# Performance work log

Measured on AMD Instinct MI355X. Metric: run time of the kernel, lower is better.

Reference implementation:

```python
import jax, jax.numpy as jnp
import numpy as np

B, C, H, W_IMG = 4, 4, 512, 512
OUT_CH = 256
POS_NUM = 512
NEG_NUM = 512
M_MARGIN = 0.5
TAU = 0.1
EPS = 1e-8


def setup_inputs() -> dict:
    key = jax.random.key(0)
    k1, k2, k3, k4, k5, k6 = jax.random.split(key, 6)
    d1_fegc = jax.random.normal(k1, (B, C, H, W_IMG), dtype=jnp.float32)
    p_fegc = jax.random.uniform(k2, (B, 1, H, W_IMG), dtype=jnp.float32)
    p_pre = jax.random.uniform(k3, (B, 3, H, W_IMG), dtype=jnp.float32)
    gt = (jax.random.uniform(k4, (B, 1, H, W_IMG)) < 0.5).astype(jnp.float32)
    # parameters of the nn.Linear(in_channel, out_channel)
    W = jax.random.normal(k5, (OUT_CH, C), dtype=jnp.float32) / np.sqrt(C)
    b_fc = jax.random.normal(k6, (OUT_CH,), dtype=jnp.float32) * 0.01
    return {"d1_fegc": d1_fegc, "p_fegc": p_fegc, "p_pre": p_pre, "gt": gt, "W": W, "b_fc": b_fc}


def _sample_idx(mask_flat, key, n):
    # randomized fixed-size sampling of n indices where mask is True
    # (replaces torch.nonzero + randperm with a jit-friendly top-k over random scores)
    score = jnp.where(mask_flat, jax.random.uniform(key, mask_flat.shape), -jnp.inf)
    _, idx = jax.lax.top_k(score, n)
    return idx


def reference(d1_fegc, p_fegc, p_pre, gt, W, b_fc):
    b, c, h, w = d1_fegc.shape
    P = POS_NUM * b
    N = NEG_NUM * b
    # p_overlap channel 3: fegc foreground AND pre argmax-class 0
    fegc_fg = p_fegc[:, 0] >= 0.5                       # [b,h,w]
    pre_cls0 = jnp.argmax(p_pre, axis=1) == 0           # [b,h,w]
    pre_region = fegc_fg & pre_cls0                     # [b,h,w]
    gt_fg = gt[:, 0] > 0.5                              # [b,h,w]
    pos_mask = (pre_region & gt_fg).reshape(-1)         # [b*h*w]
    neg_mask = (pre_region & ~gt_fg).reshape(-1)        # [b*h*w]
    # per-pixel feature vectors from d1_fegc
    feats = d1_fegc.transpose(0, 2, 3, 1).reshape(-1, c)  # [b*h*w, c]
    skey = jax.random.key(42)
    kp, kn = jax.random.split(skey)
    pos_idx = _sample_idx(pos_mask, kp, P)
    neg_idx = _sample_idx(neg_mask, kn, N)
    pts = jnp.concatenate([feats[pos_idx], feats[neg_idx]], axis=0)  # [P+N, c]
    proj = pts @ W.T + b_fc                                           # [P+N, out]
    # F.cosine_similarity with eps=1e-8 norm clamping
    norm = jnp.maximum(jnp.linalg.norm(proj, axis=-1, keepdims=True), EPS)
    normed = proj / norm
    cos_sim = normed @ normed.T                                       # [P+N, P+N]
    T = P + N
    label = jnp.ones((T, T), dtype=cos_sim.dtype)
    label = label.at[:P, P:].set(0.0).at[P:, :P].set(0.0)
    s = cos_sim / TAU
    lam = (1.0 - label) * jnp.square(s) + label * jnp.square(jnp.maximum(M_MARGIN - s, 0.0))
    lam = lam * (1.0 - jnp.eye(T, dtype=lam.dtype))                   # mask self pairs
    denom = jnp.sum(lam != 0).astype(lam.dtype)
    return jnp.sum(lam) / denom
```

## Files before the change

kernel.cpp:

```cpp
#include <hip/hip_runtime.h>
#include <stdint.h>

#define HW       262144u
#define NPIX     1048576u
#define NSEL     2048u
#define NSEG     1024u
#define SEGCAP   16u
#define DENSECAP 3584u

#define OFF_SEG     0u
#define OFF_IDX     262144u
#define OFF_VA      278528u
#define OFF_WA      360448u
#define OFF_PSUM    442368u
#define OFF_PNNZ    446464u

#define TF_ROUND(r) { x0 += x1; x1 = (x1 << (r)) | (x1 >> (32 - (r))); x1 ^= x0; }
__host__ __device__ inline void threefry2x32_(uint32_t k0, uint32_t k1,
                                              uint32_t& x0, uint32_t& x1) {
  uint32_t k2 = k0 ^ k1 ^ 0x1BD11BDAu;
  x0 += k0; x1 += k1;
  TF_ROUND(13) TF_ROUND(15) TF_ROUND(26) TF_ROUND(6)
  x0 += k1; x1 += k2 + 1u;
  TF_ROUND(17) TF_ROUND(29) TF_ROUND(16) TF_ROUND(24)
  x0 += k2; x1 += k0 + 2u;
  TF_ROUND(13) TF_ROUND(15) TF_ROUND(26) TF_ROUND(6)
  x0 += k0; x1 += k1 + 3u;
  TF_ROUND(17) TF_ROUND(29) TF_ROUND(16) TF_ROUND(24)
  x0 += k1; x1 += k2 + 4u;
  TF_ROUND(13) TF_ROUND(15) TF_ROUND(26) TF_ROUND(6)
  x0 += k2; x1 += k0 + 5u;
}

__global__ __launch_bounds__(256) void k_front(
    const float* __restrict__ pfegc, const float* __restrict__ ppre,
    const float* __restrict__ gt,
    uint32_t kp0, uint32_t kp1, uint32_t kn0, uint32_t kn1,
    uint64_t* __restrict__ seg) {
  __shared__ uint32_t cnt2[2];
  int t = threadIdx.x;
  uint32_t b = blockIdx.x;
  if (t < 2) cnt2[t] = 0;
  if (t < 2 * (int)SEGCAP) {
    uint32_t list = (uint32_t)t / SEGCAP, slot = (uint32_t)t % SEGCAP;
    seg[((size_t)list * NSEG + b) * SEGCAP + slot] = 0ull;
  }
  __syncthreads();
  uint32_t base = b * 1024u + (uint32_t)t * 4u;
  float4 pf = *(const float4*)(pfegc + base);
  float pfa[4] = { pf.x, pf.y, pf.z, pf.w };
  bool any = (pf.x >= 0.5f) || (pf.y >= 0.5f) || (pf.z >= 0.5f) || (pf.w >= 0.5f);
  if (any) {
    uint32_t hw = base & (HW - 1u);
    uint32_t bb = base >> 18;
    const float* pp = ppre + (size_t)bb * 3u * HW + hw;
    float4 p0 = *(const float4*)pp;
    float4 p1 = *(const float4*)(pp + HW);
    float4 p2 = *(const float4*)(pp + 2u * HW);
    float4 g4 = *(const float4*)(gt + base);
    float p0a[4] = { p0.x, p0.y, p0.z, p0.w };
    float p1a[4] = { p1.x, p1.y, p1.z, p1.w };
    float p2a[4] = { p2.x, p2.y, p2.z, p2.w };
    float ga[4]  = { g4.x, g4.y, g4.z, g4.w };
    #pragma unroll
    for (int j = 0; j < 4; ++j) {
      if (pfa[j] >= 0.5f && p0a[j] >= p1a[j] && p0a[j] >= p2a[j]) {
        uint32_t i = base + (uint32_t)j;
        bool gfg = ga[j] > 0.5f;
        uint32_t x0 = 0u, x1 = i;
        threefry2x32_(gfg ? kp0 : kn0, gfg ? kp1 : kn1, x0, x1);
        uint32_t r23 = (x0 ^ x1) >> 9;
        if ((r23 >> 18) == 0x1Fu) {
          uint32_t list = gfg ? 0u : 1u;
          uint32_t r = atomicAdd(&cnt2[list], 1u);
          if (r < SEGCAP)
            seg[((size_t)list * NSEG + b) * SEGCAP + r] =
                (1ull << 43) | ((uint64_t)r23 << 20) | (uint64_t)(0xFFFFFu ^ i);
        }
      }
    }
  }
}

__global__ __launch_bounds__(256) void k_sel(
    const uint64_t* __restrict__ seg, uint32_t* __restrict__ idxbuf) {
  __shared__ uint64_t dense[DENSECAP];
  __shared__ uint32_t hist[2048];
  __shared__ uint32_t part[256];
  __shared__ uint32_t skk, rank, ntot;
  __shared__ int gsel;
  __shared__ uint64_t spref;
  int t = threadIdx.x;
  int list = blockIdx.x;
  uint32_t lane = (uint32_t)t & 63u;
  if (t == 0) { spref = 0ull; skk = NSEL; rank = 0; }
  const uint4* sp4 = (const uint4*)(seg + (size_t)list * NSEG * SEGCAP);
  uint32_t c = 0;
  #pragma unroll
  for (int it = 0; it < 32; ++it) {
    uint4 v = sp4[(uint32_t)it * 256u + (uint32_t)t];
    c += ((v.y >> 11) & 1u) + ((v.w >> 11) & 1u);
  }
  part[t] = c;
  __syncthreads();
  for (int off = 1; off < 256; off <<= 1) {
    uint32_t x = part[t];
    uint32_t add = (t >= off) ? part[t - off] : 0u;
    __syncthreads();
    part[t] = x + add;
    __syncthreads();
  }
  uint32_t wbase = part[t] - c;
  if (t == 255) ntot = part[255];
  #pragma unroll
  for (int it = 0; it < 32; ++it) {
    uint4 v = sp4[(uint32_t)it * 256u + (uint32_t)t];
    uint64_t k0 = ((uint64_t)v.y << 32) | v.x;
    uint64_t k1 = ((uint64_t)v.w << 32) | v.z;
    if (k0 >> 43) { if (wbase < DENSECAP) dense[wbase] = k0; ++wbase; }
    if (k1 >> 43) { if (wbase < DENSECAP) dense[wbase] = k1; ++wbase; }
  }
  __syncthreads();
  uint32_t n = ntot; if (n > DENSECAP) n = DENSECAP;
  for (int r = 0; r < 4; ++r) {
    #pragma unroll
    for (int e = 0; e < 8; ++e) hist[t * 8 + e] = 0;
    __syncthreads();
    int csp = 44 - 11 * r;
    int cs = csp - 11;
    uint64_t pref = spref;
    for (uint32_t j = t; j < n; j += 256) {
      uint64_t key = dense[j];
      if ((key >> csp) == pref)
        atomicAdd(&hist[(uint32_t)(key >> cs) & 0x7FFu], 1u);
    }
    __syncthreads();
    uint32_t ss = 0;
    #pragma unroll
    for (int e = 0; e < 8; ++e) ss += hist[t * 8 + e];
    part[t] = ss;
    __syncthreads();
    for (int off = 1; off < 256; off <<= 1) {
      uint32_t x = part[t];
      uint32_t y = (t + off < 256) ? part[t + off] : 0u;
      __syncthreads();
      part[t] = x + y;
      __syncthreads();
    }
    uint32_t k = skk;
    if (part[t] >= k && (t == 255 || part[t + 1] < k)) gsel = t;
    __syncthreads();
    if (t == 0) {
      int g = gsel;
      uint32_t cum = (g < 255) ? part[g + 1] : 0u;
      int d = g * 8;
      for (int e = g * 8 + 7; e >= g * 8; --e) {
        uint32_t he = hist[e];
        if (cum + he >= k) { d = e; break; }
        cum += he;
      }
      skk = k - cum;
      spref = (pref << 11) | (uint64_t)(uint32_t)d;
    }
    __syncthreads();
  }
  uint64_t thr = spref;
  uint32_t niter = (n + 255u) >> 8;
  for (uint32_t it2 = 0; it2 < niter; ++it2) {
    uint32_t j = it2 * 256u + (uint32_t)t;
    uint64_t key = 0ull;
    bool v = false;
    if (j < n) { key = dense[j]; v = key >= thr; }
    unsigned long long m = __ballot(v);
    uint32_t bs = 0;
    if (lane == 0) bs = atomicAdd(&rank, (uint32_t)__popcll(m));
    bs = (uint32_t)__shfl((int)bs, 0, 64);
    if (v) {
      uint32_t s = bs + (uint32_t)__popcll(m & ((1ull << lane) - 1ull));
      if (s < NSEL)
        idxbuf[(uint32_t)list * NSEL + s] = 0xFFFFFu ^ (uint32_t)(key & 0xFFFFFu);
    }
  }
}

__global__ __launch_bounds__(256) void k_proj(
    const uint32_t* __restrict__ idxbuf, const float* __restrict__ Wm,
    const float* __restrict__ bfc, const float* __restrict__ d1,
    float* __restrict__ va, float* __restrict__ wa) {
  __shared__ float sG[25];
  __shared__ float sGw[4][25];
  int t = threadIdx.x;
  {
    float4 wr = *(const float4*)(Wm + t * 4);
    float av[5] = { wr.x, wr.y, wr.z, wr.w, bfc[t] };
    int lane = t & 63, wvi = t >> 6;
    #pragma unroll
    for (int p = 0; p < 5; ++p)
      #pragma unroll
      for (int q = p; q < 5; ++q) {
        float g = av[p] * av[q];
        #pragma unroll
        for (int off = 32; off > 0; off >>= 1)
          g += __shfl_xor(g, off, 64);
        if (lane == 0) sGw[wvi][p * 5 + q] = g;
      }
  }
  __syncthreads();
  if (t < 25) {
    int p = t / 5, q = t % 5;
    int pp = p < q ? p : q, qq = p < q ? q : p;
    sG[t] = sGw[0][pp * 5 + qq] + sGw[1][pp * 5 + qq]
          + sGw[2][pp * 5 + qq] + sGw[3][pp * 5 + qq];
  }
  __syncthreads();
  uint32_t tg = blockIdx.x * 256u + (uint32_t)t;
  uint32_t idx = idxbuf[tg] & (NPIX - 1u);
  uint32_t hw = idx & (HW - 1u);
  uint32_t bb = idx >> 18;
  const float* f = d1 + ((size_t)bb << 20) + hw;
  float y[5] = { f[0], f[HW], f[2u * HW], f[3u * HW], 1.0f };
  float z[5]; float n2 = 0.f;
  #pragma unroll
  for (int p = 0; p < 5; ++p) {
    float acc = 0.f;
    #pragma unroll
    for (int q = 0; q < 5; ++q) acc += sG[p * 5 + q] * y[q];
    z[p] = acc; n2 += acc * y[p];
  }
  n2 = fmaxf(n2, 0.f);
  float inv = 1.0f / fmaxf(sqrtf(n2), 1e-8f);
  uint32_t s5 = tg * 5u;
  #pragma unroll
  for (int p = 0; p < 5; ++p) {
    va[s5 + p] = y[p] * inv;
    wa[s5 + p] = z[p] * inv;
  }
}

__global__ __launch_bounds__(256) void k_pair(
    const float* __restrict__ va, const float* __restrict__ wa,
    float* __restrict__ psum, uint32_t* __restrict__ pnnz) {
  __shared__ float sv[128 * 5], sw[128 * 5];
  __shared__ float rs[256];
  __shared__ uint32_t rn[256];
  int i0 = blockIdx.x * 128, j0 = blockIdx.y * 128;
  int t = threadIdx.x;
  for (int u = t; u < 640; u += 256) { sv[u] = va[i0 * 5 + u]; sw[u] = wa[j0 * 5 + u]; }
  __syncthreads();
  int ty = t >> 4, tx = t & 15;
  float rv[8][5], rw[8][5];
  #pragma unroll
  for (int a = 0; a < 8; ++a)
    #pragma unroll
    for (int p = 0; p < 5; ++p) {
      rv[a][p] = sv[(ty * 8 + a) * 5 + p];
      rw[a][p] = sw[(tx * 8 + a) * 5 + p];
    }
  float lsum = 0.f; uint32_t lnz = 0;
  #pragma unroll
  for (int a = 0; a < 8; ++a) {
    int gi = i0 + ty * 8 + a;
    #pragma unroll
    for (int q = 0; q < 8; ++q) {
      int gj = j0 + tx * 8 + q;
      float c = rv[a][0]*rw[q][0] + rv[a][1]*rw[q][1] + rv[a][2]*rw[q][2]
              + rv[a][3]*rw[q][3] + rv[a][4]*rw[q][4];
      float s = c * 10.0f;
      if (gi != gj) {
        if (((gi ^ gj) & 2048) == 0) {
          float m = fmaxf(0.5f - s, 0.f);
          lsum += m * m;
          lnz += (m > 0.f) ? 1u : 0u;
        } else {
          lsum += s * s;
          lnz += (s != 0.f) ? 1u : 0u;
        }
      }
    }
  }
  rs[t] = lsum; rn[t] = lnz;
  __syncthreads();
  for (int off = 128; off > 0; off >>= 1) {
    if (t < off) { rs[t] += rs[t + off]; rn[t] += rn[t + off]; }
    __syncthreads();
  }
  if (t == 0) {
    int bid = blockIdx.y * gridDim.x + blockIdx.x;
    psum[bid] = rs[0];
    pnnz[bid] = rn[0];
  }
}

__global__ __launch_bounds__(256) void k_final(const float* __restrict__ psum,
                                               const uint32_t* __restrict__ pnnz,
                                               float* __restrict__ out) {
  __shared__ float rs[256];
  __shared__ uint32_t rn[256];
  int t = threadIdx.x;
  float s = 0.f; uint32_t nz = 0;
  for (int j = t; j < 1024; j += 256) { s += psum[j]; nz += pnnz[j]; }
  rs[t] = s; rn[t] = nz;
  __syncthreads();
  for (int off = 128; off > 0; off >>= 1) {
    if (t < off) { rs[t] += rs[t + off]; rn[t] += rn[t + off]; }
    __syncthreads();
  }
  if (t == 0) out[0] = rs[0] / (float)rn[0];
}

extern "C" void kernel_launch(void* const* d_in, const int* in_sizes, int n_in,
                              void* d_out, int out_size, void* d_ws, size_t ws_size,
                              hipStream_t stream) {
  (void)in_sizes; (void)n_in; (void)out_size; (void)ws_size;
  const float* d1    = (const float*)d_in[0];
  const float* pfegc = (const float*)d_in[1];
  const float* ppre  = (const float*)d_in[2];
  const float* gt    = (const float*)d_in[3];
  const float* W     = (const float*)d_in[4];
  const float* bfc   = (const float*)d_in[5];
  float* out = (float*)d_out;

  uint8_t* base = (uint8_t*)d_ws;
  uint64_t* seg    = (uint64_t*)(base + OFF_SEG);
  uint32_t* idxbuf = (uint32_t*)(base + OFF_IDX);
  float*    va     = (float*)(base + OFF_VA);
  float*    wa     = (float*)(base + OFF_WA);
  float*    psum   = (float*)(base + OFF_PSUM);
  uint32_t* pnnz   = (uint32_t*)(base + OFF_PNNZ);

  uint32_t kp0 = 0u, kp1 = 0u; threefry2x32_(0u, 42u, kp0, kp1);
  uint32_t kn0 = 0u, kn1 = 1u; threefry2x32_(0u, 42u, kn0, kn1);

  k_front<<<NSEG, 256, 0, stream>>>(pfegc, ppre, gt, kp0, kp1, kn0, kn1, seg);
  k_sel<<<2, 256, 0, stream>>>(seg, idxbuf);
  k_proj<<<16, 256, 0, stream>>>(idxbuf, W, bfc, d1, va, wa);
  k_pair<<<dim3(32, 32), 256, 0, stream>>>(va, wa, psum, pnnz);
  k_final<<<1, 256, 0, stream>>>(psum, pnnz, out);
}
```

Before: 124.4 us.

## Compact candidates via global atomics, single-pass select, fuse final reduction

k_front now appends sampled candidates straight into a dense global list through a global atomic counter, replacing the per-block segment buffers that k_sel had to scan and prefix-sum. k_sel keeps the keys in registers and runs a single 13-bit histogram pass plus a small exact rank among boundary-bucket keys, replacing the four-round radix select. The Gram matrix of W and b is computed once in block 0 of k_front, k_proj uses smaller blocks, and k_pair uses wave shuffles and a last-block-done atomic counter to fold in k_final. It adds a memset, contention on global atomics, and a serial O(m^2) rank step on one thread.

```diff
diff --git a/kernel.cpp b/kernel.cpp
--- a/kernel.cpp
+++ b/kernel.cpp
@@ -4,16 +4,17 @@
 #define HW       262144u
 #define NPIX     1048576u
 #define NSEL     2048u
-#define NSEG     1024u
-#define SEGCAP   16u
 #define DENSECAP 3584u
-
-#define OFF_SEG     0u
-#define OFF_IDX     262144u
-#define OFF_VA      278528u
-#define OFF_WA      360448u
-#define OFF_PSUM    442368u
-#define OFF_PNNZ    446464u
+#define SEL_PT   14u
+
+#define OFF_CNT   0u
+#define OFF_DENSE 256u
+#define OFF_IDX   57856u
+#define OFF_VA    74240u
+#define OFF_WA    156160u
+#define OFF_PSUM  238080u
+#define OFF_PNNZ  242176u
+#define OFF_G     246272u
 
 #define TF_ROUND(r) { x0 += x1; x1 = (x1 << (r)) | (x1 >> (32 - (r))); x1 ^= x0; }
 __host__ __device__ inline void threefry2x32_(uint32_t k0, uint32_t k1,
@@ -34,18 +35,14 @@
 
 __global__ __launch_bounds__(256) void k_front(
     const float* __restrict__ pfegc, const float* __restrict__ ppre,
-    const float* __restrict__ gt,
+    const float* __restrict__ gt, const float* __restrict__ Wm,
+    const float* __restrict__ bfc,
     uint32_t kp0, uint32_t kp1, uint32_t kn0, uint32_t kn1,
-    uint64_t* __restrict__ seg) {
-  __shared__ uint32_t cnt2[2];
+    uint64_t* __restrict__ dense, uint32_t* __restrict__ cnt,
+    float* __restrict__ Gout) {
+  __shared__ float sGw[4][25];
   int t = threadIdx.x;
   uint32_t b = blockIdx.x;
-  if (t < 2) cnt2[t] = 0;
-  if (t < 2 * (int)SEGCAP) {
-    uint32_t list = (uint32_t)t / SEGCAP, slot = (uint32_t)t % SEGCAP;
-    seg[((size_t)list * NSEG + b) * SEGCAP + slot] = 0ull;
-  }
-  __syncthreads();
   uint32_t base = b * 1024u + (uint32_t)t * 4u;
   float4 pf = *(const float4*)(pfegc + base);
   float pfa[4] = { pf.x, pf.y, pf.z, pf.w };
@@ -72,125 +69,15 @@
         uint32_t r23 = (x0 ^ x1) >> 9;
         if ((r23 >> 18) == 0x1Fu) {
           uint32_t list = gfg ? 0u : 1u;
-          uint32_t r = atomicAdd(&cnt2[list], 1u);
-          if (r < SEGCAP)
-            seg[((size_t)list * NSEG + b) * SEGCAP + r] =
+          uint32_t r = atomicAdd(&cnt[list], 1u);
+          if (r < DENSECAP)
+            dense[(size_t)list * DENSECAP + r] =
                 (1ull << 43) | ((uint64_t)r23 << 20) | (uint64_t)(0xFFFFFu ^ i);
         }
       }
     }
   }
-}
-
-__global__ __launch_bounds__(256) void k_sel(
-    const uint64_t* __restrict__ seg, uint32_t* __restrict__ idxbuf) {
-  __shared__ uint64_t dense[DENSECAP];
-  __shared__ uint32_t hist[2048];
-  __shared__ uint32_t part[256];
-  __shared__ uint32_t skk, rank, ntot;
-  __shared__ int gsel;
-  __shared__ uint64_t spref;
-  int t = threadIdx.x;
-  int list = blockIdx.x;
-  uint32_t lane = (uint32_t)t & 63u;
-  if (t == 0) { spref = 0ull; skk = NSEL; rank = 0; }
-  const uint4* sp4 = (const uint4*)(seg + (size_t)list * NSEG * SEGCAP);
-  uint32_t c = 0;
-  #pragma unroll
-  for (int it = 0; it < 32; ++it) {
-    uint4 v = sp4[(uint32_t)it * 256u + (uint32_t)t];
-    c += ((v.y >> 11) & 1u) + ((v.w >> 11) & 1u);
-  }
-  part[t] = c;
-  __syncthreads();
-  for (int off = 1; off < 256; off <<= 1) {
-    uint32_t x = part[t];
-    uint32_t add = (t >= off) ? part[t - off] : 0u;
-    __syncthreads();
-    part[t] = x + add;
-    __syncthreads();
-  }
-  uint32_t wbase = part[t] - c;
-  if (t == 255) ntot = part[255];
-  #pragma unroll
-  for (int it = 0; it < 32; ++it) {
-    uint4 v = sp4[(uint32_t)it * 256u + (uint32_t)t];
-    uint64_t k0 = ((uint64_t)v.y << 32) | v.x;
-    uint64_t k1 = ((uint64_t)v.w << 32) | v.z;
-    if (k0 >> 43) { if (wbase < DENSECAP) dense[wbase] = k0; ++wbase; }
-    if (k1 >> 43) { if (wbase < DENSECAP) dense[wbase] = k1; ++wbase; }
-  }
-  __syncthreads();
-  uint32_t n = ntot; if (n > DENSECAP) n = DENSECAP;
-  for (int r = 0; r < 4; ++r) {
-    #pragma unroll
-    for (int e = 0; e < 8; ++e) hist[t * 8 + e] = 0;
-    __syncthreads();
-    int csp = 44 - 11 * r;
-    int cs = csp - 11;
-    uint64_t pref = spref;
-    for (uint32_t j = t; j < n; j += 256) {
-      uint64_t key = dense[j];
-      if ((key >> csp) == pref)
-        atomicAdd(&hist[(uint32_t)(key >> cs) & 0x7FFu], 1u);
-    }
-    __syncthreads();
-    uint32_t ss = 0;
-    #pragma unroll
-    for (int e = 0; e < 8; ++e) ss += hist[t * 8 + e];
-    part[t] = ss;
-    __syncthreads();
-    for (int off = 1; off < 256; off <<= 1) {
-      uint32_t x = part[t];
-      uint32_t y = (t + off < 256) ? part[t + off] : 0u;
-      __syncthreads();
-      part[t] = x + y;
-      __syncthreads();
-    }
-    uint32_t k = skk;
-    if (part[t] >= k && (t == 255 || part[t + 1] < k)) gsel = t;
-    __syncthreads();
-    if (t == 0) {
-      int g = gsel;
-      uint32_t cum = (g < 255) ? part[g + 1] : 0u;
-      int d = g * 8;
-      for (int e = g * 8 + 7; e >= g * 8; --e) {
-        uint32_t he = hist[e];
-        if (cum + he >= k) { d = e; break; }
-        cum += he;
-      }
-      skk = k - cum;
-      spref = (pref << 11) | (uint64_t)(uint32_t)d;
-    }
-    __syncthreads();
-  }
-  uint64_t thr = spref;
-  uint32_t niter = (n + 255u) >> 8;
-  for (uint32_t it2 = 0; it2 < niter; ++it2) {
-    uint32_t j = it2 * 256u + (uint32_t)t;
-    uint64_t key = 0ull;
-    bool v = false;
-    if (j < n) { key = dense[j]; v = key >= thr; }
-    unsigned long long m = __ballot(v);
-    uint32_t bs = 0;
-    if (lane == 0) bs = atomicAdd(&rank, (uint32_t)__popcll(m));
-    bs = (uint32_t)__shfl((int)bs, 0, 64);
-    if (v) {
-      uint32_t s = bs + (uint32_t)__popcll(m & ((1ull << lane) - 1ull));
-      if (s < NSEL)
-        idxbuf[(uint32_t)list * NSEL + s] = 0xFFFFFu ^ (uint32_t)(key & 0xFFFFFu);
-    }
-  }
-}
-
-__global__ __launch_bounds__(256) void k_proj(
-    const uint32_t* __restrict__ idxbuf, const float* __restrict__ Wm,
-    const float* __restrict__ bfc, const float* __restrict__ d1,
-    float* __restrict__ va, float* __restrict__ wa) {
-  __shared__ float sG[25];
-  __shared__ float sGw[4][25];
-  int t = threadIdx.x;
-  {
+  if (b == 0) {
     float4 wr = *(const float4*)(Wm + t * 4);
     float av[5] = { wr.x, wr.y, wr.z, wr.w, bfc[t] };
     int lane = t & 63, wvi = t >> 6;
@@ -204,16 +91,114 @@
           g += __shfl_xor(g, off, 64);
         if (lane == 0) sGw[wvi][p * 5 + q] = g;
       }
-  }
-  __syncthreads();
-  if (t < 25) {
-    int p = t / 5, q = t % 5;
-    int pp = p < q ? p : q, qq = p < q ? q : p;
-    sG[t] = sGw[0][pp * 5 + qq] + sGw[1][pp * 5 + qq]
-          + sGw[2][pp * 5 + qq] + sGw[3][pp * 5 + qq];
-  }
-  __syncthreads();
-  uint32_t tg = blockIdx.x * 256u + (uint32_t)t;
+    __syncthreads();
+    if (t < 25) {
+      int p = t / 5, q = t % 5;
+      int pp = p < q ? p : q, qq = p < q ? q : p;
+      Gout[t] = sGw[0][pp * 5 + qq] + sGw[1][pp * 5 + qq]
+              + sGw[2][pp * 5 + qq] + sGw[3][pp * 5 + qq];
+    }
+  }
+}
+
+__global__ __launch_bounds__(256) void k_sel(
+    const uint64_t* __restrict__ dense, const uint32_t* __restrict__ cnt,
+    uint32_t* __restrict__ idxbuf) {
+  __shared__ uint32_t hist[8192];
+  __shared__ uint64_t bnd[128];
+  __shared__ uint32_t wsum[4];
+  __shared__ uint32_t bcnt, rank, sb, sneed;
+  __shared__ uint64_t sthr;
+  int t = threadIdx.x;
+  int list = blockIdx.x;
+  uint32_t lane = (uint32_t)t & 63u, wv = (uint32_t)t >> 6;
+  if (t == 0) { bcnt = 0u; rank = 0u; sb = 0u; sneed = 1u; }
+  uint32_t n = cnt[list];
+  if (n > DENSECAP) n = DENSECAP;
+  const uint64_t* dp = dense + (size_t)list * DENSECAP;
+  uint64_t kreg[SEL_PT];
+  #pragma unroll
+  for (uint32_t r = 0; r < SEL_PT; ++r) {
+    uint32_t j = r * 256u + (uint32_t)t;
+    kreg[r] = (j < n) ? dp[j] : 0ull;
+  }
+  #pragma unroll
+  for (int e = 0; e < 32; ++e) hist[t * 32 + e] = 0u;
+  __syncthreads();
+  #pragma unroll
+  for (uint32_t r = 0; r < SEL_PT; ++r)
+    if (kreg[r]) atomicAdd(&hist[(uint32_t)(kreg[r] >> 25) & 8191u], 1u);
+  __syncthreads();
+  uint32_t s = 0;
+  #pragma unroll
+  for (int e = 0; e < 32; ++e) s += hist[t * 32 + e];
+  uint32_t suf = s;
+  #pragma unroll
+  for (int off = 1; off < 64; off <<= 1) {
+    uint32_t v = (uint32_t)__shfl_down((int)suf, off, 64);
+    if (lane + (uint32_t)off < 64u) suf += v;
+  }
+  if (lane == 0) wsum[wv] = suf;
+  __syncthreads();
+  uint32_t wafter = 0;
+  for (uint32_t u = wv + 1u; u < 4u; ++u) wafter += wsum[u];
+  uint32_t after_t = wafter + (suf - s);
+  if (after_t < NSEL && after_t + s >= NSEL) {
+    uint32_t running = after_t;
+    for (int e = 31; e >= 0; --e) {
+      uint32_t h = hist[t * 32 + e];
+      running += h;
+      if (running >= NSEL) { sb = (uint32_t)(t * 32 + e); sneed = NSEL - (running - h); break; }
+    }
+  }
+  __syncthreads();
+  uint32_t b_star = sb, need = sneed;
+  #pragma unroll
+  for (uint32_t r = 0; r < SEL_PT; ++r) {
+    uint64_t k = kreg[r];
+    if (k && ((uint32_t)(k >> 25) & 8191u) == b_star) {
+      uint32_t p = atomicAdd(&bcnt, 1u);
+      if (p < 128u) bnd[p] = k;
+    }
+  }
+  __syncthreads();
+  if (t == 0) {
+    uint32_t m = bcnt; if (m > 128u) m = 128u;
+    uint64_t thr = bnd[0];
+    for (uint32_t i = 0; i < m; ++i) {
+      uint32_t rk = 1u;
+      for (uint32_t j = 0; j < m; ++j) rk += (bnd[j] > bnd[i]) ? 1u : 0u;
+      if (rk == need) { thr = bnd[i]; break; }
+    }
+    sthr = thr;
+  }
+  __syncthreads();
+  uint64_t thr = sthr;
+  #pragma unroll
+  for (uint32_t r = 0; r < SEL_PT; ++r) {
+    uint64_t k = kreg[r];
+    bool v = (k != 0ull) && (k >= thr);
+    unsigned long long mb = __ballot(v);
+    uint32_t bs = 0;
+    if (lane == 0) bs = atomicAdd(&rank, (uint32_t)__popcll(mb));
+    bs = (uint32_t)__shfl((int)bs, 0, 64);
+    if (v) {
+      uint32_t s2 = bs + (uint32_t)__popcll(mb & ((1ull << lane) - 1ull));
+      if (s2 < NSEL)
+        idxbuf[(uint32_t)list * NSEL + s2] = 0xFFFFFu ^ (uint32_t)(k & 0xFFFFFu);
+    }
+  }
+}
+
+__global__ __launch_bounds__(64) void k_proj(
+    const uint32_t* __restrict__ idxbuf, const float* __restrict__ Gin,
+    const float* __restrict__ d1,
+    float* __restrict__ va, float* __restrict__ wa) {
+  __shared__ float sG[25];
+  int t = threadIdx.x;
+  if (t < 25) sG[t] = Gin[t];
+  __syncthreads();
+  uint32_t tg = blockIdx.x * 64u + (uint32_t)t;
   uint32_t idx = idxbuf[tg] & (NPIX - 1u);
   uint32_t hw = idx & (HW - 1u);
   uint32_t bb = idx >> 18;
@@ -239,13 +224,19 @@
 
 __global__ __launch_bounds__(256) void k_pair(
     const float* __restrict__ va, const float* __restrict__ wa,
-    float* __restrict__ psum, uint32_t* __restrict__ pnnz) {
-  __shared__ float sv[128 * 5], sw[128 * 5];
-  __shared__ float rs[256];
-  __shared__ uint32_t rn[256];
+    float* __restrict__ psum, uint32_t* __restrict__ pnnz,
+    uint32_t* __restrict__ done, float* __restrict__ out) {
+  __shared__ __align__(16) float sv[640], sw[640];
+  __shared__ float wps[4];
+  __shared__ uint32_t wpn[4];
+  __shared__ uint32_t isl;
   int i0 = blockIdx.x * 128, j0 = blockIdx.y * 128;
   int t = threadIdx.x;
-  for (int u = t; u < 640; u += 256) { sv[u] = va[i0 * 5 + u]; sw[u] = wa[j0 * 5 + u]; }
+  int lane = t & 63, wv = t >> 6;
+  if (t < 160) {
+    ((float4*)sv)[t] = ((const float4*)(va + i0 * 5))[t];
+    ((float4*)sw)[t] = ((const float4*)(wa + j0 * 5))[t];
+  }
   __syncthreads();
   int ty = t >> 4, tx = t & 15;
   float rv[8][5], rw[8][5];
@@ -265,47 +256,53 @@
       int gj = j0 + tx * 8 + q;
       float c = rv[a][0]*rw[q][0] + rv[a][1]*rw[q][1] + rv[a][2]*rw[q][2]
               + rv[a][3]*rw[q][3] + rv[a][4]*rw[q][4];
-      float s = c * 10.0f;
+      float sc = c * 10.0f;
       if (gi != gj) {
         if (((gi ^ gj) & 2048) == 0) {
-          float m = fmaxf(0.5f - s, 0.f);
+          float m = fmaxf(0.5f - sc, 0.f);
           lsum += m * m;
           lnz += (m > 0.f) ? 1u : 0u;
         } else {
-          lsum += s * s;
-          lnz += (s != 0.f) ? 1u : 0u;
+          lsum += sc * sc;
+          lnz += (sc != 0.f) ? 1u : 0u;
         }
       }
     }
   }
-  rs[t] = lsum; rn[t] = lnz;
-  __syncthreads();
-  for (int off = 128; off > 0; off >>= 1) {
-    if (t < off) { rs[t] += rs[t + off]; rn[t] += rn[t + off]; }
+  #pragma unroll
+  for (int off = 32; off > 0; off >>= 1) {
+    lsum += __shfl_xor(lsum, off, 64);
+    lnz  += (uint32_t)__shfl_xor((int)lnz, off, 64);
+  }
+  if (lane == 0) { wps[wv] = lsum; wpn[wv] = lnz; }
+  __syncthreads();
+  if (t == 0) {
+    float s = wps[0] + wps[1] + wps[2] + wps[3];
+    uint32_t nz = wpn[0] + wpn[1] + wpn[2] + wpn[3];
+    int bid = blockIdx.y * (int)gridDim.x + blockIdx.x;
+    __hip_atomic_store(&psum[bid], s, __ATOMIC_RELEASE, __HIP_MEMORY_SCOPE_AGENT);
+    __hip_atomic_store(&pnnz[bid], nz, __ATOMIC_RELEASE, __HIP_MEMORY_SCOPE_AGENT);
+    uint32_t v = __hip_atomic_fetch_add(done, 1u, __ATOMIC_ACQ_REL, __HIP_MEMORY_SCOPE_AGENT);
+    isl = (v == 1023u) ? 1u : 0u;
+  }
+  __syncthreads();
+  if (isl) {
+    float s = 0.f; uint32_t nz = 0u;
+    for (int j = t; j < 1024; j += 256) {
+      s  += __hip_atomic_load(&psum[j], __ATOMIC_RELAXED, __HIP_MEMORY_SCOPE_AGENT);
+      nz += __hip_atomic_load(&pnnz[j], __ATOMIC_RELAXED, __HIP_MEMORY_SCOPE_AGENT);
+    }
+    #pragma unroll
+    for (int off = 32; off > 0; off >>= 1) {
+      s  += __shfl_xor(s, off, 64);
+      nz += (uint32_t)__shfl_xor((int)nz, off, 64);
+    }
+    if (lane == 0) { wps[wv] = s; wpn[wv] = nz; }
     __syncthreads();
-  }
-  if (t == 0) {
-    int bid = blockIdx.y * gridDim.x + blockIdx.x;
-    psum[bid] = rs[0];
-    pnnz[bid] = rn[0];
-  }
-}
-
-__global__ __launch_bounds__(256) void k_final(const float* __restrict__ psum,
-                                               const uint32_t* __restrict__ pnnz,
-                                               float* __restrict__ out) {
-  __shared__ float rs[256];
-  __shared__ uint32_t rn[256];
-  int t = threadIdx.x;
-  float s = 0.f; uint32_t nz = 0;
-  for (int j = t; j < 1024; j += 256) { s += psum[j]; nz += pnnz[j]; }
-  rs[t] = s; rn[t] = nz;
-  __syncthreads();
-  for (int off = 128; off > 0; off >>= 1) {
-    if (t < off) { rs[t] += rs[t + off]; rn[t] += rn[t + off]; }
-    __syncthreads();
-  }
-  if (t == 0) out[0] = rs[0] / (float)rn[0];
+    if (t == 0)
+      out[0] = (wps[0] + wps[1] + wps[2] + wps[3])
+             / (float)(wpn[0] + wpn[1] + wpn[2] + wpn[3]);
+  }
 }
 
 extern "C" void kernel_launch(void* const* d_in, const int* in_sizes, int n_in,
@@ -321,19 +318,22 @@
   float* out = (float*)d_out;
 
   uint8_t* base = (uint8_t*)d_ws;
-  uint64_t* seg    = (uint64_t*)(base + OFF_SEG);
+  uint32_t* cnt    = (uint32_t*)(base + OFF_CNT);
+  uint64_t* dense  = (uint64_t*)(base + OFF_DENSE);
   uint32_t* idxbuf = (uint32_t*)(base + OFF_IDX);
   float*    va     = (float*)(base + OFF_VA);
   float*    wa     = (float*)(base + OFF_WA);
   float*    psum   = (float*)(base + OFF_PSUM);
   uint32_t* pnnz   = (uint32_t*)(base + OFF_PNNZ);
+  float*    Gws    = (float*)(base + OFF_G);
 
   uint32_t kp0 = 0u, kp1 = 0u; threefry2x32_(0u, 42u, kp0, kp1);
   uint32_t kn0 = 0u, kn1 = 1u; threefry2x32_(0u, 42u, kn0, kn1);
 
-  k_front<<<NSEG, 256, 0, stream>>>(pfegc, ppre, gt, kp0, kp1, kn0, kn1, seg);
-  k_sel<<<2, 256, 0, stream>>>(seg, idxbuf);
-  k_proj<<<16, 256, 0, stream>>>(idxbuf, W, bfc, d1, va, wa);
-  k_pair<<<dim3(32, 32), 256, 0, stream>>>(va, wa, psum, pnnz);
-  k_final<<<1, 256, 0, stream>>>(psum, pnnz, out);
-}
+  hipMemsetAsync(base + OFF_CNT, 0, 16, stream);
+  k_front<<<1024, 256, 0, stream>>>(pfegc, ppre, gt, W, bfc,
+                                    kp0, kp1, kn0, kn1, dense, cnt, Gws);
+  k_sel<<<2, 256, 0, stream>>>(dense, cnt, idxbuf);
+  k_proj<<<64, 64, 0, stream>>>(idxbuf, Gws, d1, va, wa);
+  k_pair<<<dim3(32, 32), 256, 0, stream>>>(va, wa, psum, pnnz, cnt + 2, out);
+}
```

Measured after the change: 196.8 us. 58.2% more time.
